# Kernel tuning notes

Hardware: AMD Instinct MI355X
Metric: run time of the kernel (lower is better)

The kernel has to match this reference:

```python
import jax, jax.numpy as jnp
import numpy as np

E = 64          # num_experts
TOPK = 8        # num_experts_per_tok
I = 512         # moe_intermediate_size
H = 1024        # hidden_size
G = 128         # awq group_size
T = 2048        # tokens (batch*seq)

# AWQ nibble unpack order: bit shifts [0,16,4,20,8,24,12,28] -> indices [0,4,1,5,2,6,3,7]
_AWQ_SHIFTS = jnp.array([0, 4, 1, 5, 2, 6, 3, 7], dtype=jnp.int32) * 4


def awq_dequant(qw, qz, scales, group_size=G):
    """qw: (K, N//8) int32, qz: (K//G, N//8) int32, scales: (K//G, N) float.
    Returns dense weight (K, N): (q - z) * scale with per-group zero/scale."""
    K = qw.shape[0]
    uq = ((qw[:, :, None] >> _AWQ_SHIFTS) & 0xF).reshape(K, -1)          # (K, N)
    uz = ((qz[:, :, None] >> _AWQ_SHIFTS) & 0xF).reshape(qz.shape[0], -1)  # (K//G, N)
    uz = jnp.repeat(uz, group_size, axis=0)                               # (K, N)
    sc = jnp.repeat(scales, group_size, axis=0)                           # (K, N)
    return (uq.astype(scales.dtype) - uz.astype(scales.dtype)) * sc


def setup_inputs() -> dict:
    key = jax.random.key(0)
    ks = jax.random.split(key, 8)
    imax = 2**31 - 1
    return {
        "x": jax.random.normal(ks[0], (T, H), dtype=jnp.float32),
        "gate_w": jax.random.normal(ks[1], (E, H), dtype=jnp.float32) * 0.02,
        "qweight1": jax.random.randint(ks[2], (H, (E * I) // 8), 0, imax, dtype=jnp.int32),
        "qzeros1": jax.random.randint(ks[3], (H // G, (E * I) // 8), 0, imax, dtype=jnp.int32),
        "scales1": jax.random.normal(ks[4], (H // G, E * I), dtype=jnp.float32) * 0.02,
        "qweight2": jax.random.randint(ks[5], (I, (E * H) // 8), 0, imax, dtype=jnp.int32),
        "qzeros2": jax.random.randint(ks[6], (I // G, (E * H) // 8), 0, imax, dtype=jnp.int32),
        "scales2": jax.random.normal(ks[7], (I // G, E * H), dtype=jnp.float32) * 0.02,
    }


def reference(x, gate_w, qweight1, qzeros1, scales1, qweight2, qzeros2, scales2):
    # dequant grouped expert weights
    w1 = awq_dequant(qweight1, qzeros1, scales1).T.reshape(E, I, H)   # (E, I, H)
    w2 = awq_dequant(qweight2, qzeros2, scales2).T.reshape(E, H, I)   # (E, H, I)

    # routing: softmax -> top-k -> renormalize
    logits = x @ gate_w.T                                             # (T, E)
    probs = jax.nn.softmax(logits, axis=-1)
    topv, topi = jax.lax.top_k(probs, TOPK)                           # (T, K)
    topv = topv / jnp.sum(topv, axis=-1, keepdims=True)
    cw = jnp.sum(jax.nn.one_hot(topi, E, dtype=x.dtype) * topv[..., None], axis=1)  # (T, E)

    # experts: out = sum_e cw[t,e] * silu(x @ w1[e].T) @ w2[e].T
    h = jax.nn.silu(jnp.einsum('th,eih->tei', x, w1))                 # (T, E, I)
    h = h * cw[:, :, None]                                            # fold combine weights
    out = jnp.einsum('tei,ehi->th', h, w2)                            # (T, H)
    return out
```

## Files before the change

### kernel.cpp

```cpp
#include <hip/hip_runtime.h>
#include <hip/hip_bf16.h>

#define T_TOK 2048
#define HID   1024
#define EXP   64
#define TOPK  8
#define IMED  512
#define N1 (EXP * IMED)
#define C1 (N1 / 8)
#define N2 (EXP * HID)
#define C2 (N2 / 8)

typedef _Float16 h16x2 __attribute__((ext_vector_type(2)));
typedef _Float16 h16x8 __attribute__((ext_vector_type(8)));
typedef float f32x4 __attribute__((ext_vector_type(4)));
typedef unsigned short ushortx4 __attribute__((ext_vector_type(4)));
typedef unsigned short ushortx8 __attribute__((ext_vector_type(8)));

__constant__ int kShifts[8] = {0, 16, 4, 20, 8, 24, 12, 28};

__device__ __forceinline__ void async16(const void* g, void* l) {
  __builtin_amdgcn_global_load_lds((const __attribute__((address_space(1))) void*)g,
                                   (__attribute__((address_space(3))) void*)l, 16, 0, 0);
}

__device__ __forceinline__ unsigned short f2h(float f) {
  return __builtin_bit_cast(unsigned short, (_Float16)f);
}
__device__ __forceinline__ float h2f(unsigned short b) {
  return (float)__builtin_bit_cast(_Float16, b);
}

__device__ __forceinline__ h16x8 unpack8h(unsigned q, h16x2 sh2, h16x2 zh2) {
  union { unsigned u[4]; h16x8 v; } out;
#pragma unroll
  for (int j = 0; j < 4; ++j) {
    const unsigned m = ((q >> (4 * j)) & 0x000F000Fu) | 0x64006400u;
    h16x2 d = __builtin_bit_cast(h16x2, m) - zh2;
    d = d * sh2;
    out.u[j] = __builtin_bit_cast(unsigned, d);
  }
  return out.v;
}

__global__ __launch_bounds__(256) void cast_x_kernel(const float* __restrict__ x,
                                                     unsigned short* __restrict__ xh) {
  const int i = (blockIdx.x * 256 + threadIdx.x) * 4;
  float4 v = *reinterpret_cast<const float4*>(x + i);
  ushortx4 o;
  o[0] = f2h(v.x); o[1] = f2h(v.y); o[2] = f2h(v.z); o[3] = f2h(v.w);
  *reinterpret_cast<ushortx4*>(xh + i) = o;
}

__global__ __launch_bounds__(256) void logits_f32_kernel(
    const float* __restrict__ x, const float* __restrict__ gate_w,
    float* __restrict__ partial) {
  const int t0 = blockIdx.x * 64;
  const int k0 = blockIdx.y * 128;
  const int tid = threadIdx.x;

  __shared__ float xs[64][128];
  __shared__ float gs[64][128];

  const int lrow = tid >> 5;
  const int cblk = tid & 31;
#pragma unroll
  for (int r = 0; r < 8; ++r) {
    const int row = r * 8 + lrow;
    const int sc = (cblk ^ ((row >> 2) & 7)) * 4;
    float4 xv = *reinterpret_cast<const float4*>(x + (size_t)(t0 + row) * HID + k0 + cblk * 4);
    float4 gv = *reinterpret_cast<const float4*>(gate_w + (size_t)row * HID + k0 + cblk * 4);
    *reinterpret_cast<float4*>(&xs[row][sc]) = xv;
    *reinterpret_cast<float4*>(&gs[row][sc]) = gv;
  }
  __syncthreads();

  const int tg = (tid >> 4) * 4;
  const int eg = (tid & 15) * 4;
  const int xsw = (tid >> 4) & 7;
  const int gsw = tid & 7;
  float acc[4][4] = {{0.f}};
#pragma unroll 8
  for (int k = 0; k < 128; k += 4) {
    const int c = k >> 2;
    float4 a[4], b[4];
#pragma unroll
    for (int i = 0; i < 4; ++i)
      a[i] = *reinterpret_cast<const float4*>(&xs[tg + i][(c ^ xsw) * 4]);
#pragma unroll
    for (int j = 0; j < 4; ++j)
      b[j] = *reinterpret_cast<const float4*>(&gs[eg + j][(c ^ gsw) * 4]);
#pragma unroll
    for (int i = 0; i < 4; ++i)
#pragma unroll
      for (int j = 0; j < 4; ++j) {
        acc[i][j] = fmaf(a[i].x, b[j].x, acc[i][j]);
        acc[i][j] = fmaf(a[i].y, b[j].y, acc[i][j]);
        acc[i][j] = fmaf(a[i].z, b[j].z, acc[i][j]);
        acc[i][j] = fmaf(a[i].w, b[j].w, acc[i][j]);
      }
  }
  float* dst = partial + ((size_t)blockIdx.y * T_TOK + t0) * EXP;
#pragma unroll
  for (int i = 0; i < 4; ++i)
    *reinterpret_cast<float4*>(dst + (tg + i) * EXP + eg) =
        make_float4(acc[i][0], acc[i][1], acc[i][2], acc[i][3]);
}

__global__ __launch_bounds__(256) void topk_kernel(
    const float* __restrict__ partial, int* __restrict__ counts,
    int* __restrict__ tok_list, int* __restrict__ hslot_list,
    float* __restrict__ cw_list) {
  const int wave = threadIdx.x >> 6, lane = threadIdx.x & 63;
  const int t = blockIdx.x * 4 + wave;
  float lg = 0.f;
#pragma unroll
  for (int s = 0; s < 8; ++s)
    lg += partial[((size_t)s * T_TOK + t) * EXP + lane];

  float m = lg;
  for (int off = 32; off; off >>= 1) m = fmaxf(m, __shfl_xor(m, off));
  float pe = expf(lg - m);
  float s = pe;
  for (int off = 32; off; off >>= 1) s += __shfl_xor(s, off);
  float prob = pe / s;

  float pcur = prob;
  float myv = 0.f;
  int myi = -1;
  float tsum = 0.f;
  for (int k = 0; k < TOPK; ++k) {
    float vv = pcur;
    int idx = lane;
    for (int off = 32; off; off >>= 1) {
      float ov = __shfl_xor(vv, off);
      int oi = __shfl_xor(idx, off);
      if (ov > vv || (ov == vv && oi < idx)) { vv = ov; idx = oi; }
    }
    tsum += vv;
    if (lane == k) { myv = vv; myi = idx; }
    if (lane == idx) pcur = -1.f;
  }

  if (lane < TOPK) {
    const float cw = myv / tsum;
    const int ex = myi;
    const int slot = atomicAdd(&counts[ex], 1);
    tok_list[ex * T_TOK + slot] = t;
    hslot_list[ex * T_TOK + slot] = t * TOPK + lane;
    cw_list[ex * T_TOK + slot] = cw;
  }
}

__global__ __launch_bounds__(256) void repack_kernel(
    const int* __restrict__ qw, unsigned* __restrict__ qk, int K, int C) {
  const int pp = blockIdx.y;
  const int t = pp >> 2, fq = pp & 3;
  const int c2 = blockIdx.x * 512 + threadIdx.x * 2;
  const int nblk = c2 >> 1;
  unsigned o0[16], o1[16];
#pragma unroll
  for (int i = 0; i < 16; ++i) { o0[i] = 0u; o1[i] = 0u; }
  const int k0a = t * 64 + fq * 8;
  const int k0b = t * 64 + (fq + 4) * 8;
#pragma unroll
  for (int r = 0; r < 8; ++r) {
    const int2 va = *reinterpret_cast<const int2*>(qw + (size_t)(k0a + r) * C + c2);
    const int2 vb = *reinterpret_cast<const int2*>(qw + (size_t)(k0b + r) * C + c2);
    const int outsh = (r & 1) * 16 + (r >> 1) * 4;
    const unsigned qa[2] = {(unsigned)va.x, (unsigned)va.y};
    const unsigned qb[2] = {(unsigned)vb.x, (unsigned)vb.y};
#pragma unroll
    for (int ci = 0; ci < 2; ++ci) {
#pragma unroll
      for (int j = 0; j < 8; ++j) {
        const int sh = kShifts[j];
        o0[ci * 8 + j] |= ((qa[ci] >> sh) & 0xFu) << outsh;
        o1[ci * 8 + j] |= ((qb[ci] >> sh) & 0xFu) << outsh;
      }
    }
  }
  unsigned* dst = qk + (size_t)nblk * 2 * K + t * 128 + fq * 32;
#pragma unroll
  for (int idx = 0; idx < 16; ++idx)
    *reinterpret_cast<uint2*>(dst + idx * 2) = make_uint2(o0[idx], o1[idx]);
}

__global__ __launch_bounds__(256) void mfma_gemm1(
    const unsigned short* __restrict__ xh, const unsigned* __restrict__ qk1,
    const int* __restrict__ qz1, const float* __restrict__ sc1,
    const int* __restrict__ counts, const int* __restrict__ tok_list,
    const int* __restrict__ hslot_list, const float* __restrict__ cw_list,
    unsigned short* __restrict__ h_buf) {
  const int e = blockIdx.z;
  const int n_e = counts[e];
  const int t0 = blockIdx.y * 64;
  if (t0 >= n_e) return;
  const int ntile = blockIdx.x;
  const int tid = threadIdx.x;
  const int wave = tid >> 6, lane = tid & 63;
  const int fr = lane & 15, fq = lane >> 4;

  __shared__ unsigned short As[2][64 * 64];

  const int arow = tid >> 3;
  const int acb = ((tid & 7) ^ ((tid >> 3) & 7)) * 16;
  const int ta0 = tok_list[e * T_TOK + min(t0 + arow, n_e - 1)];
  const int ta1 = tok_list[e * T_TOK + min(t0 + 32 + arow, n_e - 1)];
  const char* ga0 = (const char*)(xh + (size_t)ta0 * HID) + acb;
  const char* ga1 = (const char*)(xh + (size_t)ta1 * HID) + acb;

  auto stage = [&](int b) {
    char* l = (char*)&As[b][0] + wave * 1024;
    async16(ga0, l);
    async16(ga1, l + 4096);
    ga0 += 128; ga1 += 128;
  };

  const int nbase = e * IMED + ntile * 64 + wave * 16;
  const unsigned* bp = qk1 + (size_t)(nbase >> 4) * (2 * HID) + fq * 32 + fr * 2;
  const int col = nbase + fr;
  const int shz = ((fr >> 1) & 3) * 4 + (fr & 1) * 16;

  f32x4 acc[4];
#pragma unroll
  for (int i = 0; i < 4; ++i) acc[i] = (f32x4){0.f, 0.f, 0.f, 0.f};

  stage(0);
  uint2 qcur = *reinterpret_cast<const uint2*>(bp);
  float s_cur = sc1[col];
  unsigned zd_cur = (unsigned)qz1[col >> 3];
  int p = 0;
#pragma unroll 1
  for (int g = 0; g < HID / 128; ++g) {
    const unsigned shb = (unsigned)f2h(s_cur);
    const h16x2 sh2 = __builtin_bit_cast(h16x2, shb | (shb << 16));
    const unsigned zb = 0x6400u | ((zd_cur >> shz) & 15u);
    const h16x2 zh2 = __builtin_bit_cast(h16x2, zb | (zb << 16));
    float s_nxt = 0.f; unsigned zd_nxt = 0u;
#pragma unroll
    for (int hh = 0; hh < 2; ++hh) {
      const int t = g * 2 + hh;
      __syncthreads();
      if (t + 1 < HID / 64) stage(p ^ 1);
      uint2 qnext = make_uint2(0u, 0u);
      if (t + 1 < HID / 64) qnext = *reinterpret_cast<const uint2*>(bp + (t + 1) * 128);
      if (hh == 1 && g + 1 < HID / 128) {
        s_nxt = sc1[(size_t)(g + 1) * N1 + col];
        zd_nxt = (unsigned)qz1[(size_t)(g + 1) * C1 + (col >> 3)];
      }
      const h16x8 b0 = unpack8h(qcur.x, sh2, zh2);
      const h16x8 b1 = unpack8h(qcur.y, sh2, zh2);
#pragma unroll
      for (int kk = 0; kk < 2; ++kk) {
        const h16x8 bb = kk ? b1 : b0;
#pragma unroll
        for (int i = 0; i < 4; ++i) {
          const int row = i * 16 + fr;
          const h16x8 a = *reinterpret_cast<const h16x8*>(
              &As[p][row * 64 + (((kk * 4 + fq) ^ (fr & 7)) * 8)]);
          acc[i] = __builtin_amdgcn_mfma_f32_16x16x32_f16(a, bb, acc[i], 0, 0, 0);
        }
      }
      qcur = qnext; p ^= 1;
    }
    s_cur = s_nxt; zd_cur = zd_nxt;
  }

#pragma unroll
  for (int i = 0; i < 4; ++i) {
#pragma unroll
    for (int r = 0; r < 4; ++r) {
      const int grow = t0 + i * 16 + fq * 4 + r;
      if (grow < n_e) {
        const float cw = cw_list[e * T_TOK + grow];
        const int hs = hslot_list[e * T_TOK + grow];
        const float v = acc[i][r];
        h_buf[(size_t)hs * IMED + ntile * 64 + wave * 16 + fr] =
            f2h((v / (1.f + expf(-v))) * cw);
      }
    }
  }
}

__global__ __launch_bounds__(256) void mfma_gemm2(
    const unsigned short* __restrict__ h_buf, const unsigned* __restrict__ qk2,
    const int* __restrict__ qz2, const float* __restrict__ sc2,
    const int* __restrict__ counts, const int* __restrict__ hslot_list,
    unsigned short* __restrict__ p_buf) {
  const int e = blockIdx.z;
  const int n_e = counts[e];
  const int t0 = blockIdx.y * 64;
  if (t0 >= n_e) return;
  const int ntile = blockIdx.x;
  const int tid = threadIdx.x;
  const int wave = tid >> 6, lane = tid & 63;
  const int fr = lane & 15, fq = lane >> 4;

  __shared__ unsigned short As[2][64 * 64];

  const int arow = tid >> 3;
  const int acb = ((tid & 7) ^ ((tid >> 3) & 7)) * 16;
  const int ha0 = hslot_list[e * T_TOK + min(t0 + arow, n_e - 1)];
  const int ha1 = hslot_list[e * T_TOK + min(t0 + 32 + arow, n_e - 1)];
  const char* ga0 = (const char*)(h_buf + (size_t)ha0 * IMED) + acb;
  const char* ga1 = (const char*)(h_buf + (size_t)ha1 * IMED) + acb;

  auto stage = [&](int b) {
    char* l = (char*)&As[b][0] + wave * 1024;
    async16(ga0, l);
    async16(ga1, l + 4096);
    ga0 += 128; ga1 += 128;
  };

  const int nbase = e * HID + ntile * 64 + wave * 16;
  const unsigned* bp = qk2 + (size_t)(nbase >> 4) * (2 * IMED) + fq * 32 + fr * 2;
  const int col = nbase + fr;
  const int shz = ((fr >> 1) & 3) * 4 + (fr & 1) * 16;

  f32x4 acc[4];
#pragma unroll
  for (int i = 0; i < 4; ++i) acc[i] = (f32x4){0.f, 0.f, 0.f, 0.f};

  stage(0);
  uint2 qcur = *reinterpret_cast<const uint2*>(bp);
  float s_cur = sc2[col];
  unsigned zd_cur = (unsigned)qz2[col >> 3];
  int p = 0;
#pragma unroll 1
  for (int g = 0; g < IMED / 128; ++g) {
    const unsigned shb = (unsigned)f2h(s_cur);
    const h16x2 sh2 = __builtin_bit_cast(h16x2, shb | (shb << 16));
    const unsigned zb = 0x6400u | ((zd_cur >> shz) & 15u);
    const h16x2 zh2 = __builtin_bit_cast(h16x2, zb | (zb << 16));
    float s_nxt = 0.f; unsigned zd_nxt = 0u;
#pragma unroll
    for (int hh = 0; hh < 2; ++hh) {
      const int t = g * 2 + hh;
      __syncthreads();
      if (t + 1 < IMED / 64) stage(p ^ 1);
      uint2 qnext = make_uint2(0u, 0u);
      if (t + 1 < IMED / 64) qnext = *reinterpret_cast<const uint2*>(bp + (t + 1) * 128);
      if (hh == 1 && g + 1 < IMED / 128) {
        s_nxt = sc2[(size_t)(g + 1) * N2 + col];
        zd_nxt = (unsigned)qz2[(size_t)(g + 1) * C2 + (col >> 3)];
      }
      const h16x8 b0 = unpack8h(qcur.x, sh2, zh2);
      const h16x8 b1 = unpack8h(qcur.y, sh2, zh2);
#pragma unroll
      for (int kk = 0; kk < 2; ++kk) {
        const h16x8 bb = kk ? b1 : b0;
#pragma unroll
        for (int i = 0; i < 4; ++i) {
          const int row = i * 16 + fr;
          const h16x8 a = *reinterpret_cast<const h16x8*>(
              &As[p][row * 64 + (((kk * 4 + fq) ^ (fr & 7)) * 8)]);
          acc[i] = __builtin_amdgcn_mfma_f32_16x16x32_f16(a, bb, acc[i], 0, 0, 0);
        }
      }
      qcur = qnext; p ^= 1;
    }
    s_cur = s_nxt; zd_cur = zd_nxt;
  }

#pragma unroll
  for (int i = 0; i < 4; ++i) {
#pragma unroll
    for (int r = 0; r < 4; ++r) {
      const int grow = t0 + i * 16 + fq * 4 + r;
      if (grow < n_e) {
        const int hs = hslot_list[e * T_TOK + grow];
        p_buf[(size_t)hs * HID + ntile * 64 + wave * 16 + fr] = f2h(acc[i][r]);
      }
    }
  }
}

__global__ __launch_bounds__(256) void reduce_kernel(const unsigned short* __restrict__ p_buf,
                                                     float* __restrict__ out) {
  const int idx = blockIdx.x * 256 + threadIdx.x;
  const int t = idx >> 7;
  const int c0 = (idx & 127) * 8;
  float s[8] = {0.f, 0.f, 0.f, 0.f, 0.f, 0.f, 0.f, 0.f};
#pragma unroll
  for (int k = 0; k < TOPK; ++k) {
    ushortx8 v = *reinterpret_cast<const ushortx8*>(p_buf + ((size_t)t * TOPK + k) * HID + c0);
#pragma unroll
    for (int j = 0; j < 8; ++j) s[j] += h2f(v[j]);
  }
  float* dst = out + (size_t)t * HID + c0;
  *reinterpret_cast<float4*>(dst) = make_float4(s[0], s[1], s[2], s[3]);
  *reinterpret_cast<float4*>(dst + 4) = make_float4(s[4], s[5], s[6], s[7]);
}

extern "C" void kernel_launch(void* const* d_in, const int* in_sizes, int n_in,
                              void* d_out, int out_size, void* d_ws, size_t ws_size,
                              hipStream_t stream) {
  const float* x      = (const float*)d_in[0];
  const float* gate_w = (const float*)d_in[1];
  const int*   qw1    = (const int*)d_in[2];
  const int*   qz1    = (const int*)d_in[3];
  const float* sc1    = (const float*)d_in[4];
  const int*   qw2    = (const int*)d_in[5];
  const int*   qz2    = (const int*)d_in[6];
  const float* sc2    = (const float*)d_in[7];
  float* out = (float*)d_out;

  char* ws = (char*)d_ws;
  int* counts           = (int*)(ws);
  int* tok_list         = (int*)(ws + 256);
  int* hslot_list       = (int*)(ws + 524544);
  float* cw_list        = (float*)(ws + 1048832);
  unsigned short* h_buf = (unsigned short*)(ws + 1573120);
  unsigned short* xh    = (unsigned short*)(ws + 18350336);
  unsigned* qk1         = (unsigned*)(ws + 22544640);
  unsigned* qk2         = (unsigned*)(ws + 39321856);
  unsigned short* p_buf = (unsigned short*)(ws + 56099072);
  float* partial        = (float*)(ws + 89653504);

  hipMemsetAsync(counts, 0, 256, stream);

  cast_x_kernel<<<(T_TOK * HID / 4) / 256, 256, 0, stream>>>(x, xh);
  logits_f32_kernel<<<dim3(T_TOK / 64, HID / 128), 256, 0, stream>>>(x, gate_w, partial);
  topk_kernel<<<T_TOK / 4, 256, 0, stream>>>(partial, counts, tok_list, hslot_list, cw_list);
  repack_kernel<<<dim3(C1 / 512, HID / 16), 256, 0, stream>>>(qw1, qk1, HID, C1);
  repack_kernel<<<dim3(C2 / 512, IMED / 16), 256, 0, stream>>>(qw2, qk2, IMED, C2);

  mfma_gemm1<<<dim3(IMED / 64, T_TOK / 64, EXP), 256, 0, stream>>>(
      xh, qk1, qz1, sc1, counts, tok_list, hslot_list, cw_list, h_buf);
  mfma_gemm2<<<dim3(HID / 64, T_TOK / 64, EXP), 256, 0, stream>>>(
      h_buf, qk2, qz2, sc2, counts, hslot_list, p_buf);
  reduce_kernel<<<(T_TOK * HID / 8) / 256, 256, 0, stream>>>(p_buf, out);
}
```

Before: 254.5 us.

## Fuse cast, router logits and weight repack into one prep kernel; widen GEMM token tiles

```diff
diff --git a/kernel.cpp b/kernel.cpp
--- a/kernel.cpp
+++ b/kernel.cpp
@@ -43,68 +43,102 @@
   return out.v;
 }
 
-__global__ __launch_bounds__(256) void cast_x_kernel(const float* __restrict__ x,
-                                                     unsigned short* __restrict__ xh) {
-  const int i = (blockIdx.x * 256 + threadIdx.x) * 4;
-  float4 v = *reinterpret_cast<const float4*>(x + i);
-  ushortx4 o;
-  o[0] = f2h(v.x); o[1] = f2h(v.y); o[2] = f2h(v.z); o[3] = f2h(v.w);
-  *reinterpret_cast<ushortx4*>(xh + i) = o;
-}
-
-__global__ __launch_bounds__(256) void logits_f32_kernel(
+__device__ __forceinline__ void repack_body(const int* __restrict__ qw,
+                                            unsigned* __restrict__ qk, int K, int C,
+                                            int gx, int pp, int tid) {
+  const int t = pp >> 2, fq = pp & 3;
+  const int c2 = gx * 512 + tid * 2;
+  const int nblk = c2 >> 1;
+  unsigned o0[16], o1[16];
+#pragma unroll
+  for (int i = 0; i < 16; ++i) { o0[i] = 0u; o1[i] = 0u; }
+  const int k0a = t * 64 + fq * 8;
+  const int k0b = t * 64 + (fq + 4) * 8;
+#pragma unroll
+  for (int r = 0; r < 8; ++r) {
+    const int2 va = *reinterpret_cast<const int2*>(qw + (size_t)(k0a + r) * C + c2);
+    const int2 vb = *reinterpret_cast<const int2*>(qw + (size_t)(k0b + r) * C + c2);
+    const int outsh = (r & 1) * 16 + (r >> 1) * 4;
+    const unsigned qa[2] = {(unsigned)va.x, (unsigned)va.y};
+    const unsigned qb[2] = {(unsigned)vb.x, (unsigned)vb.y};
+#pragma unroll
+    for (int ci = 0; ci < 2; ++ci) {
+#pragma unroll
+      for (int j = 0; j < 8; ++j) {
+        const int sh = kShifts[j];
+        o0[ci * 8 + j] |= ((qa[ci] >> sh) & 0xFu) << outsh;
+        o1[ci * 8 + j] |= ((qb[ci] >> sh) & 0xFu) << outsh;
+      }
+    }
+  }
+  unsigned* dst = qk + (size_t)nblk * 2 * K + t * 128 + fq * 32;
+#pragma unroll
+  for (int idx = 0; idx < 16; ++idx)
+    *reinterpret_cast<uint2*>(dst + idx * 2) = make_uint2(o0[idx], o1[idx]);
+}
+
+__global__ __launch_bounds__(256) void prep_kernel(
     const float* __restrict__ x, const float* __restrict__ gate_w,
-    float* __restrict__ partial) {
-  const int t0 = blockIdx.x * 64;
-  const int k0 = blockIdx.y * 128;
+    unsigned short* __restrict__ xh, float* __restrict__ partial,
+    const int* __restrict__ qw1, unsigned* __restrict__ qk1,
+    const int* __restrict__ qw2, unsigned* __restrict__ qk2) {
+  const int bid = blockIdx.x;
   const int tid = threadIdx.x;
-
-  __shared__ float xs[64][128];
-  __shared__ float gs[64][128];
-
-  const int lrow = tid >> 5;
-  const int cblk = tid & 31;
-#pragma unroll
-  for (int r = 0; r < 8; ++r) {
-    const int row = r * 8 + lrow;
-    const int sc = (cblk ^ ((row >> 2) & 7)) * 4;
-    float4 xv = *reinterpret_cast<const float4*>(x + (size_t)(t0 + row) * HID + k0 + cblk * 4);
-    float4 gv = *reinterpret_cast<const float4*>(gate_w + (size_t)row * HID + k0 + cblk * 4);
-    *reinterpret_cast<float4*>(&xs[row][sc]) = xv;
-    *reinterpret_cast<float4*>(&gs[row][sc]) = gv;
-  }
-  __syncthreads();
-
-  const int tg = (tid >> 4) * 4;
-  const int eg = (tid & 15) * 4;
-  const int xsw = (tid >> 4) & 7;
-  const int gsw = tid & 7;
-  float acc[4][4] = {{0.f}};
-#pragma unroll 8
-  for (int k = 0; k < 128; k += 4) {
-    const int c = k >> 2;
-    float4 a[4], b[4];
+  if (bid < 512) {
+    __shared__ float xs[64][64];
+    __shared__ float gs[64][64];
+    const int t0 = (bid & 31) * 64;
+    const int ks = bid >> 5;
+    const int k0 = ks * 64;
+    const int lrow = tid >> 4;
+    const int cblk = tid & 15;
+#pragma unroll
+    for (int r = 0; r < 4; ++r) {
+      const int row = r * 16 + lrow;
+      const int sc = (cblk ^ ((row >> 2) & 15)) * 4;
+      float4 xv = *reinterpret_cast<const float4*>(x + (size_t)(t0 + row) * HID + k0 + cblk * 4);
+      float4 gv = *reinterpret_cast<const float4*>(gate_w + (size_t)row * HID + k0 + cblk * 4);
+      *reinterpret_cast<float4*>(&xs[row][sc]) = xv;
+      *reinterpret_cast<float4*>(&gs[row][sc]) = gv;
+      ushortx4 o;
+      o[0] = f2h(xv.x); o[1] = f2h(xv.y); o[2] = f2h(xv.z); o[3] = f2h(xv.w);
+      *reinterpret_cast<ushortx4*>(xh + (size_t)(t0 + row) * HID + k0 + cblk * 4) = o;
+    }
+    __syncthreads();
+    const int tg = (tid >> 4) * 4, eg = (tid & 15) * 4;
+    const int xsw = tid >> 4, gsw = tid & 15;
+    float acc[4][4] = {{0.f, 0.f, 0.f, 0.f}};
+#pragma unroll 4
+    for (int c = 0; c < 16; ++c) {
+      float4 a[4], b[4];
+#pragma unroll
+      for (int i = 0; i < 4; ++i)
+        a[i] = *reinterpret_cast<const float4*>(&xs[tg + i][(c ^ xsw) * 4]);
+#pragma unroll
+      for (int j = 0; j < 4; ++j)
+        b[j] = *reinterpret_cast<const float4*>(&gs[eg + j][(c ^ gsw) * 4]);
+#pragma unroll
+      for (int i = 0; i < 4; ++i)
+#pragma unroll
+        for (int j = 0; j < 4; ++j) {
+          acc[i][j] = fmaf(a[i].x, b[j].x, acc[i][j]);
+          acc[i][j] = fmaf(a[i].y, b[j].y, acc[i][j]);
+          acc[i][j] = fmaf(a[i].z, b[j].z, acc[i][j]);
+          acc[i][j] = fmaf(a[i].w, b[j].w, acc[i][j]);
+        }
+    }
+    float* dst = partial + ((size_t)ks * T_TOK + t0) * EXP;
 #pragma unroll
     for (int i = 0; i < 4; ++i)
-      a[i] = *reinterpret_cast<const float4*>(&xs[tg + i][(c ^ xsw) * 4]);
-#pragma unroll
-    for (int j = 0; j < 4; ++j)
-      b[j] = *reinterpret_cast<const float4*>(&gs[eg + j][(c ^ gsw) * 4]);
-#pragma unroll
-    for (int i = 0; i < 4; ++i)
-#pragma unroll
-      for (int j = 0; j < 4; ++j) {
-        acc[i][j] = fmaf(a[i].x, b[j].x, acc[i][j]);
-        acc[i][j] = fmaf(a[i].y, b[j].y, acc[i][j]);
-        acc[i][j] = fmaf(a[i].z, b[j].z, acc[i][j]);
-        acc[i][j] = fmaf(a[i].w, b[j].w, acc[i][j]);
-      }
-  }
-  float* dst = partial + ((size_t)blockIdx.y * T_TOK + t0) * EXP;
-#pragma unroll
-  for (int i = 0; i < 4; ++i)
-    *reinterpret_cast<float4*>(dst + (tg + i) * EXP + eg) =
-        make_float4(acc[i][0], acc[i][1], acc[i][2], acc[i][3]);
+      *reinterpret_cast<float4*>(dst + (tg + i) * EXP + eg) =
+          make_float4(acc[i][0], acc[i][1], acc[i][2], acc[i][3]);
+  } else if (bid < 1024) {
+    const int id = bid - 512;
+    repack_body(qw1, qk1, HID, C1, id & 7, id >> 3, tid);
+  } else {
+    const int id = bid - 1024;
+    repack_body(qw2, qk2, IMED, C2, id & 15, id >> 4, tid);
+  }
 }
 
 __global__ __launch_bounds__(256) void topk_kernel(
@@ -115,7 +149,7 @@
   const int t = blockIdx.x * 4 + wave;
   float lg = 0.f;
 #pragma unroll
-  for (int s = 0; s < 8; ++s)
+  for (int s = 0; s < 16; ++s)
     lg += partial[((size_t)s * T_TOK + t) * EXP + lane];
 
   float m = lg;
@@ -152,40 +186,6 @@
   }
 }
 
-__global__ __launch_bounds__(256) void repack_kernel(
-    const int* __restrict__ qw, unsigned* __restrict__ qk, int K, int C) {
-  const int pp = blockIdx.y;
-  const int t = pp >> 2, fq = pp & 3;
-  const int c2 = blockIdx.x * 512 + threadIdx.x * 2;
-  const int nblk = c2 >> 1;
-  unsigned o0[16], o1[16];
-#pragma unroll
-  for (int i = 0; i < 16; ++i) { o0[i] = 0u; o1[i] = 0u; }
-  const int k0a = t * 64 + fq * 8;
-  const int k0b = t * 64 + (fq + 4) * 8;
-#pragma unroll
-  for (int r = 0; r < 8; ++r) {
-    const int2 va = *reinterpret_cast<const int2*>(qw + (size_t)(k0a + r) * C + c2);
-    const int2 vb = *reinterpret_cast<const int2*>(qw + (size_t)(k0b + r) * C + c2);
-    const int outsh = (r & 1) * 16 + (r >> 1) * 4;
-    const unsigned qa[2] = {(unsigned)va.x, (unsigned)va.y};
-    const unsigned qb[2] = {(unsigned)vb.x, (unsigned)vb.y};
-#pragma unroll
-    for (int ci = 0; ci < 2; ++ci) {
-#pragma unroll
-      for (int j = 0; j < 8; ++j) {
-        const int sh = kShifts[j];
-        o0[ci * 8 + j] |= ((qa[ci] >> sh) & 0xFu) << outsh;
-        o1[ci * 8 + j] |= ((qb[ci] >> sh) & 0xFu) << outsh;
-      }
-    }
-  }
-  unsigned* dst = qk + (size_t)nblk * 2 * K + t * 128 + fq * 32;
-#pragma unroll
-  for (int idx = 0; idx < 16; ++idx)
-    *reinterpret_cast<uint2*>(dst + idx * 2) = make_uint2(o0[idx], o1[idx]);
-}
-
 __global__ __launch_bounds__(256) void mfma_gemm1(
     const unsigned short* __restrict__ xh, const unsigned* __restrict__ qk1,
     const int* __restrict__ qz1, const float* __restrict__ sc1,
@@ -194,27 +194,39 @@
     unsigned short* __restrict__ h_buf) {
   const int e = blockIdx.z;
   const int n_e = counts[e];
-  const int t0 = blockIdx.y * 64;
+  const int t0 = blockIdx.y * 128;
   if (t0 >= n_e) return;
   const int ntile = blockIdx.x;
   const int tid = threadIdx.x;
   const int wave = tid >> 6, lane = tid & 63;
   const int fr = lane & 15, fq = lane >> 4;
 
-  __shared__ unsigned short As[2][64 * 64];
+  __shared__ unsigned short As[2][128 * 64];
 
   const int arow = tid >> 3;
-  const int acb = ((tid & 7) ^ ((tid >> 3) & 7)) * 16;
-  const int ta0 = tok_list[e * T_TOK + min(t0 + arow, n_e - 1)];
-  const int ta1 = tok_list[e * T_TOK + min(t0 + 32 + arow, n_e - 1)];
-  const char* ga0 = (const char*)(xh + (size_t)ta0 * HID) + acb;
-  const char* ga1 = (const char*)(xh + (size_t)ta1 * HID) + acb;
+  const int acb = ((tid & 7) ^ (arow & 7)) * 16;
+  const char* ga0;
+  const char* ga1;
+  const char* ga2;
+  const char* ga3;
+  {
+    const int ta0 = tok_list[e * T_TOK + min(t0 + arow, n_e - 1)];
+    const int ta1 = tok_list[e * T_TOK + min(t0 + 32 + arow, n_e - 1)];
+    const int ta2 = tok_list[e * T_TOK + min(t0 + 64 + arow, n_e - 1)];
+    const int ta3 = tok_list[e * T_TOK + min(t0 + 96 + arow, n_e - 1)];
+    ga0 = (const char*)(xh + (size_t)ta0 * HID) + acb;
+    ga1 = (const char*)(xh + (size_t)ta1 * HID) + acb;
+    ga2 = (const char*)(xh + (size_t)ta2 * HID) + acb;
+    ga3 = (const char*)(xh + (size_t)ta3 * HID) + acb;
+  }
 
   auto stage = [&](int b) {
     char* l = (char*)&As[b][0] + wave * 1024;
     async16(ga0, l);
     async16(ga1, l + 4096);
-    ga0 += 128; ga1 += 128;
+    async16(ga2, l + 8192);
+    async16(ga3, l + 12288);
+    ga0 += 128; ga1 += 128; ga2 += 128; ga3 += 128;
   };
 
   const int nbase = e * IMED + ntile * 64 + wave * 16;
@@ -222,9 +234,9 @@
   const int col = nbase + fr;
   const int shz = ((fr >> 1) & 3) * 4 + (fr & 1) * 16;
 
-  f32x4 acc[4];
-#pragma unroll
-  for (int i = 0; i < 4; ++i) acc[i] = (f32x4){0.f, 0.f, 0.f, 0.f};
+  f32x4 acc[8];
+#pragma unroll
+  for (int i = 0; i < 8; ++i) acc[i] = (f32x4){0.f, 0.f, 0.f, 0.f};
 
   stage(0);
   uint2 qcur = *reinterpret_cast<const uint2*>(bp);
@@ -255,7 +267,7 @@
       for (int kk = 0; kk < 2; ++kk) {
         const h16x8 bb = kk ? b1 : b0;
 #pragma unroll
-        for (int i = 0; i < 4; ++i) {
+        for (int i = 0; i < 8; ++i) {
           const int row = i * 16 + fr;
           const h16x8 a = *reinterpret_cast<const h16x8*>(
               &As[p][row * 64 + (((kk * 4 + fq) ^ (fr & 7)) * 8)]);
@@ -268,7 +280,7 @@
   }
 
 #pragma unroll
-  for (int i = 0; i < 4; ++i) {
+  for (int i = 0; i < 8; ++i) {
 #pragma unroll
     for (int r = 0; r < 4; ++r) {
       const int grow = t0 + i * 16 + fq * 4 + r;
@@ -290,27 +302,39 @@
     unsigned short* __restrict__ p_buf) {
   const int e = blockIdx.z;
   const int n_e = counts[e];
-  const int t0 = blockIdx.y * 64;
+  const int t0 = blockIdx.y * 128;
   if (t0 >= n_e) return;
   const int ntile = blockIdx.x;
   const int tid = threadIdx.x;
   const int wave = tid >> 6, lane = tid & 63;
   const int fr = lane & 15, fq = lane >> 4;
 
-  __shared__ unsigned short As[2][64 * 64];
+  __shared__ unsigned short As[2][128 * 64];
 
   const int arow = tid >> 3;
-  const int acb = ((tid & 7) ^ ((tid >> 3) & 7)) * 16;
-  const int ha0 = hslot_list[e * T_TOK + min(t0 + arow, n_e - 1)];
-  const int ha1 = hslot_list[e * T_TOK + min(t0 + 32 + arow, n_e - 1)];
-  const char* ga0 = (const char*)(h_buf + (size_t)ha0 * IMED) + acb;
-  const char* ga1 = (const char*)(h_buf + (size_t)ha1 * IMED) + acb;
+  const int acb = ((tid & 7) ^ (arow & 7)) * 16;
+  const char* ga0;
+  const char* ga1;
+  const char* ga2;
+  const char* ga3;
+  {
+    const int ha0 = hslot_list[e * T_TOK + min(t0 + arow, n_e - 1)];
+    const int ha1 = hslot_list[e * T_TOK + min(t0 + 32 + arow, n_e - 1)];
+    const int ha2 = hslot_list[e * T_TOK + min(t0 + 64 + arow, n_e - 1)];
+    const int ha3 = hslot_list[e * T_TOK + min(t0 + 96 + arow, n_e - 1)];
+    ga0 = (const char*)(h_buf + (size_t)ha0 * IMED) + acb;
+    ga1 = (const char*)(h_buf + (size_t)ha1 * IMED) + acb;
+    ga2 = (const char*)(h_buf + (size_t)ha2 * IMED) + acb;
+    ga3 = (const char*)(h_buf + (size_t)ha3 * IMED) + acb;
+  }
 
   auto stage = [&](int b) {
     char* l = (char*)&As[b][0] + wave * 1024;
     async16(ga0, l);
     async16(ga1, l + 4096);
-    ga0 += 128; ga1 += 128;
+    async16(ga2, l + 8192);
+    async16(ga3, l + 12288);
+    ga0 += 128; ga1 += 128; ga2 += 128; ga3 += 128;
   };
 
   const int nbase = e * HID + ntile * 64 + wave * 16;
@@ -318,9 +342,9 @@
   const int col = nbase + fr;
   const int shz = ((fr >> 1) & 3) * 4 + (fr & 1) * 16;
 
-  f32x4 acc[4];
-#pragma unroll
-  for (int i = 0; i < 4; ++i) acc[i] = (f32x4){0.f, 0.f, 0.f, 0.f};
+  f32x4 acc[8];
+#pragma unroll
+  for (int i = 0; i < 8; ++i) acc[i] = (f32x4){0.f, 0.f, 0.f, 0.f};
 
   stage(0);
   uint2 qcur = *reinterpret_cast<const uint2*>(bp);
@@ -351,7 +375,7 @@
       for (int kk = 0; kk < 2; ++kk) {
         const h16x8 bb = kk ? b1 : b0;
 #pragma unroll
-        for (int i = 0; i < 4; ++i) {
+        for (int i = 0; i < 8; ++i) {
           const int row = i * 16 + fr;
           const h16x8 a = *reinterpret_cast<const h16x8*>(
               &As[p][row * 64 + (((kk * 4 + fq) ^ (fr & 7)) * 8)]);
@@ -364,7 +388,7 @@
   }
 
 #pragma unroll
-  for (int i = 0; i < 4; ++i) {
+  for (int i = 0; i < 8; ++i) {
 #pragma unroll
     for (int r = 0; r < 4; ++r) {
       const int grow = t0 + i * 16 + fq * 4 + r;
@@ -420,15 +444,12 @@
 
   hipMemsetAsync(counts, 0, 256, stream);
 
-  cast_x_kernel<<<(T_TOK * HID / 4) / 256, 256, 0, stream>>>(x, xh);
-  logits_f32_kernel<<<dim3(T_TOK / 64, HID / 128), 256, 0, stream>>>(x, gate_w, partial);
+  prep_kernel<<<1536, 256, 0, stream>>>(x, gate_w, xh, partial, qw1, qk1, qw2, qk2);
   topk_kernel<<<T_TOK / 4, 256, 0, stream>>>(partial, counts, tok_list, hslot_list, cw_list);
-  repack_kernel<<<dim3(C1 / 512, HID / 16), 256, 0, stream>>>(qw1, qk1, HID, C1);
-  repack_kernel<<<dim3(C2 / 512, IMED / 16), 256, 0, stream>>>(qw2, qk2, IMED, C2);
-
-  mfma_gemm1<<<dim3(IMED / 64, T_TOK / 64, EXP), 256, 0, stream>>>(
+
+  mfma_gemm1<<<dim3(IMED / 64, T_TOK / 128, EXP), 256, 0, stream>>>(
       xh, qk1, qz1, sc1, counts, tok_list, hslot_list, cw_list, h_buf);
-  mfma_gemm2<<<dim3(HID / 64, T_TOK / 64, EXP), 256, 0, stream>>>(
+  mfma_gemm2<<<dim3(HID / 64, T_TOK / 128, EXP), 256, 0, stream>>>(
       h_buf, qk2, qz2, sc2, counts, hslot_list, p_buf);
   reduce_kernel<<<(T_TOK * HID / 8) / 256, 256, 0, stream>>>(p_buf, out);
 }
```

After: 270.0 us. 6.1% more time.
